# Optimization experiments

Measured on AMD Instinct MI355X. Metric: run time of the kernel, lower is better.

Reference implementation:

```python
import jax, jax.numpy as jnp
import numpy as np

N, E, F = 25000, 200000, 128


def setup_inputs() -> dict:
    key = jax.random.key(0)
    k1, k2, k3, k4 = jax.random.split(key, 4)
    x = jax.random.normal(k1, (N, F), dtype=jnp.float32)
    edge_index = jax.random.randint(k2, (2, E), 0, N, dtype=jnp.int32)
    batch = jnp.zeros((N,), dtype=jnp.int32)  # single graph
    # EdgePooling.lin = Linear(2F, 1); split weight into src/dst halves
    w_src = jax.random.normal(k3, (F,), dtype=jnp.float32) / np.sqrt(2.0 * F)
    w_dst = jax.random.normal(k4, (F,), dtype=jnp.float32) / np.sqrt(2.0 * F)
    b = jnp.zeros((1,), dtype=jnp.float32)
    return {"x": x, "edge_index": edge_index, "batch": batch,
            "w_src": w_src, "w_dst": w_dst, "b": b}


def reference(x, edge_index, batch, w_src, w_dst, b):
    src, dst = edge_index[0], edge_index[1]
    n = x.shape[0]
    # raw edge score: lin(cat(x[src], x[dst])) == x[src]@w_src + x[dst]@w_dst + b
    raw = x[src] @ w_src + x[dst] @ w_dst + b[0]                 # [E]
    # compute_edge_score_softmax: softmax over edges grouped by dst node
    m = jax.ops.segment_max(raw, dst, num_segments=n)
    z = jnp.exp(raw - m[dst])
    denom = jax.ops.segment_sum(z, dst, num_segments=n)
    e = z / denom[dst] + 0.5                                      # add_to_edge_score=0.5

    # greedy non-overlapping edge contraction, highest score first
    order = jnp.argsort(-e)
    src_s, dst_s, e_s = src[order], dst[order], e[order]

    def step(carry, st):
        matched, cluster, cnt = carry
        s, t = st
        ok = jnp.logical_not(matched[s] | matched[t])
        matched = matched.at[s].set(matched[s] | ok)
        matched = matched.at[t].set(matched[t] | ok)
        cluster = cluster.at[s].set(jnp.where(ok, cnt, cluster[s]))
        cluster = cluster.at[t].set(jnp.where(ok, cnt, cluster[t]))
        out = (ok, jnp.where(ok, cnt, n))  # n = sentinel (dropped later)
        cnt = cnt + ok.astype(cnt.dtype)
        return (matched, cluster, cnt), out

    init = (jnp.zeros((n,), bool), jnp.zeros((n,), jnp.int32), jnp.int32(0))
    (matched, cluster, cnt), (chosen, assigned) = jax.lax.scan(step, init, (src_s, dst_s))

    # leftover (unmatched) nodes become singleton clusters with consecutive ids
    left = jnp.logical_not(matched)
    cluster = jnp.where(left, cnt + jnp.cumsum(left.astype(jnp.int32)) - 1, cluster)
    num_clusters = cnt + left.sum()

    # per-cluster gating score: merged-edge score for pairs, 1.0 for singletons
    cscore = jnp.ones((n,), x.dtype).at[assigned].set(e_s, mode='drop')
    # new node features (padded to n rows; rows >= num_clusters are zero)
    new_x = jax.ops.segment_sum(x, cluster, num_segments=n) * cscore[:, None]
    new_batch = jnp.zeros((n,), batch.dtype).at[cluster].set(batch)
    new_ei = cluster[edge_index]
    new_ei = jnp.where(new_ei[0] == new_ei[1], -1, new_ei)  # mark self-loops invalid
    return new_x, new_ei, new_batch, num_clusters
```

## Files before the change

### kernel.cpp

```cpp
#include <hip/hip_runtime.h>
#include <stdint.h>

typedef unsigned int u32;
typedef unsigned long long u64;
typedef unsigned short u16;
typedef unsigned char u8;

#define FDIM  128
#define NNODE 25000
#define WG    1024
#define RB    64
#define EPT   16
#define RCHUNK (RB*EPT)
#define KBITS 18
#define RMASK ((1u << KBITS) - 1u)
#define TAG(r) (((0x3FFFu - (u32)(r)) << KBITS))
#define PRROUNDS 4
#define CB 256
#define CEPT 4
#define CCHUNK (CB*CEPT)
#define HST (256*200)
#define SCCH 1024

__device__ __forceinline__ u32 enc_f32(float f){
  u32 u = __float_as_uint(f);
  return (u & 0x80000000u) ? ~u : (u | 0x80000000u);
}
__device__ __forceinline__ float dec_f32(u32 u){
  u = (u & 0x80000000u) ? (u ^ 0x80000000u) : ~u;
  return __uint_as_float(u);
}

__device__ __forceinline__ float xla_expf(float x){
  x = fminf(x,  88.3762626647950f);
  x = fmaxf(x, -88.3762626647949f);
  float fx = floorf(fmaf(x, 1.44269504088896341f, 0.5f));
  float tmp = __fmul_rn(fx, 0.693359375f);
  float zz  = __fmul_rn(fx, -2.12194440e-4f);
  x = __fsub_rn(x, tmp);
  x = __fsub_rn(x, zz);
  float z2 = __fmul_rn(x, x);
  float y = fmaf(1.9875691500E-4f, x, 1.3981999507E-3f);
  y = fmaf(y, x, 8.3334519073E-3f);
  y = fmaf(y, x, 4.1665795894E-2f);
  y = fmaf(y, x, 1.6666665459E-1f);
  y = fmaf(y, x, 5.0000001201E-1f);
  y = fmaf(y, z2, x);
  y = __fadd_rn(y, 1.0f);
  int n = (int)fx;
  float p2n = __uint_as_float((u32)(n + 127) << 23);
  return __fmul_rn(y, p2n);
}

__global__ __launch_bounds__(256) void k_dots(const float* __restrict__ x,
                      const float* __restrict__ wsrc, const float* __restrict__ wdst,
                      float* __restrict__ ds, float* __restrict__ dd, int N_)
{
  __shared__ float4 w4[64];
  int t = threadIdx.x;
  if (t < 32) w4[t] = ((const float4*)wsrc)[t];
  else if (t < 64) w4[t] = ((const float4*)wdst)[t - 32];
  __syncthreads();
  int v = blockIdx.x * blockDim.x + t;
  if (v >= N_) return;
  const float4* xr = (const float4*)(x + (size_t)v * FDIM);
  float accs = 0.f, accd = 0.f;
  #pragma unroll 4
  for (int k = 0; k < 32; ++k) {
    float4 xv = xr[k], w = w4[k], u = w4[k + 32];
    accs = __fadd_rn(accs, __fmul_rn(xv.x, w.x));
    accs = __fadd_rn(accs, __fmul_rn(xv.y, w.y));
    accs = __fadd_rn(accs, __fmul_rn(xv.z, w.z));
    accs = __fadd_rn(accs, __fmul_rn(xv.w, w.w));
    accd = __fadd_rn(accd, __fmul_rn(xv.x, u.x));
    accd = __fadd_rn(accd, __fmul_rn(xv.y, u.y));
    accd = __fadd_rn(accd, __fmul_rn(xv.z, u.z));
    accd = __fadd_rn(accd, __fmul_rn(xv.w, u.w));
  }
  ds[v] = accs; dd[v] = accd;
}

__global__ __launch_bounds__(RB) void k_rawE(const int* __restrict__ ei, const float* __restrict__ ds,
                       const float* __restrict__ dd, const float* __restrict__ bia,
                       float* __restrict__ raw, u32* __restrict__ m_enc,
                       u64* __restrict__ kvA, u32* __restrict__ hist, int nb, int E_)
{
  __shared__ u32 h[256];
  int t = threadIdx.x, b = blockIdx.x;
  for (int i = t; i < 256; i += RB) h[i] = 0;
  __syncthreads();
  int lo = b * RCHUNK + t * EPT;
  int hi = lo + EPT; if (hi > E_) hi = E_;
  float bv = bia[0];
  for (int e = lo; e < hi; ++e) {
    int s = ei[e], d = ei[E_ + e];
    float r = __fadd_rn(__fadd_rn(ds[s], dd[d]), bv);
    raw[e] = r;
    atomicMax(&m_enc[d], enc_f32(r));
    kvA[e] = ((u64)(u32)d << 32) | (u32)e;
    atomicAdd(&h[(u32)d & 255u], 1u);
  }
  __syncthreads();
  for (int i = t; i < 256; i += RB) hist[(size_t)i * nb + b] = h[i];
}

__global__ __launch_bounds__(RB) void k_rhist(const u64* __restrict__ kv, u32* __restrict__ hist,
                                              int n, int nb, int shift)
{
  __shared__ u32 h[256];
  int t = threadIdx.x, b = blockIdx.x;
  for (int i = t; i < 256; i += RB) h[i] = 0;
  __syncthreads();
  int lo = b * RCHUNK + t * EPT;
  int hi = lo + EPT; if (hi > n) hi = n;
  for (int i = lo; i < hi; ++i) atomicAdd(&h[((u32)(kv[i] >> 32) >> shift) & 255u], 1u);
  __syncthreads();
  for (int i = t; i < 256; i += RB) hist[(size_t)i * nb + b] = h[i];
}

__global__ __launch_bounds__(256) void k_mbs1(const u32* __restrict__ a, u32* __restrict__ bsum, int m)
{
  __shared__ u32 sh[256];
  int t = threadIdx.x, b = blockIdx.x;
  int base = b * SCCH;
  u32 s = 0;
  #pragma unroll
  for (int k = 0; k < SCCH / 256; ++k) { int i = base + t + k * 256; if (i < m) s += a[i]; }
  sh[t] = s; __syncthreads();
  for (int off = 128; off > 0; off >>= 1) { if (t < off) sh[t] += sh[t + off]; __syncthreads(); }
  if (t == 0) bsum[b] = sh[0];
}

__global__ __launch_bounds__(256) void k_mbs3(u32* __restrict__ a, const u32* __restrict__ bsum, int m)
{
  __shared__ u32 sh[256];
  __shared__ u32 s_off;
  const int W = SCCH / 256;
  int t = threadIdx.x, b = blockIdx.x;
  sh[t] = (t < b) ? bsum[t] : 0u;
  __syncthreads();
  for (int off = 128; off > 0; off >>= 1) { if (t < off) sh[t] += sh[t + off]; __syncthreads(); }
  if (t == 0) s_off = sh[0];
  __syncthreads();
  int lo = b * SCCH + t * W;
  u32 v[W];
  u32 c = 0;
  #pragma unroll
  for (int k = 0; k < W; ++k) { int i = lo + k; v[k] = (i < m) ? a[i] : 0u; c += v[k]; }
  u32 mine = c;
  sh[t] = c; __syncthreads();
  for (int off = 1; off < 256; off <<= 1) {
    u32 x = (t >= off) ? sh[t - off] : 0u; __syncthreads();
    sh[t] += x; __syncthreads();
  }
  u32 run = s_off + sh[t] - mine;
  #pragma unroll
  for (int k = 0; k < W; ++k) { int i = lo + k; if (i < m) { a[i] = run; run += v[k]; } }
}

__global__ __launch_bounds__(RB) void k_rscat(const u64* __restrict__ kvin, u64* __restrict__ kvout,
                                              const u32* __restrict__ base, int n, int nb, int shift)
{
  __shared__ u16 h[RB][258];
  __shared__ u32 gbase[256];
  int t = threadIdx.x, b = blockIdx.x;
  for (int i = t; i < RB * 258 / 2; i += RB) ((u32*)h)[i] = 0u;
  __syncthreads();
  int lo = b * RCHUNK + t * EPT;
  int hi = lo + EPT; if (hi > n) hi = n;
  for (int i = lo; i < hi; ++i) { u32 d = ((u32)(kvin[i] >> 32) >> shift) & 255u; h[t][d]++; }
  __syncthreads();
  for (int dg = t; dg < 256; dg += RB) {
    u32 run = 0;
    for (int q = 0; q < RB; ++q) { u16 c = h[q][dg]; h[q][dg] = (u16)run; run += c; }
    gbase[dg] = base[(size_t)dg * nb + b];
  }
  __syncthreads();
  for (int i = lo; i < hi; ++i) {
    u64 kv = kvin[i];
    u32 d = ((u32)(kv >> 32) >> shift) & 255u;
    u32 p = gbase[d] + (u32)h[t][d];
    h[t][d]++;
    kvout[p] = kv;
  }
}

__global__ __launch_bounds__(RB) void k_rscatP(const u64* __restrict__ kvin,
                                               const u32* __restrict__ base, int n, int nb, int shift,
                                               u32* __restrict__ pairByRank, float* __restrict__ scoreByRank,
                                               u8* __restrict__ chosen, u32* __restrict__ nmin)
{
  __shared__ u16 h[RB][258];
  __shared__ u32 gbase[256];
  int t = threadIdx.x, b = blockIdx.x;
  for (int i = t; i < RB * 258 / 2; i += RB) ((u32*)h)[i] = 0u;
  __syncthreads();
  int lo = b * RCHUNK + t * EPT;
  int hi = lo + EPT; if (hi > n) hi = n;
  for (int i = lo; i < hi; ++i) { u32 d = ((u32)(kvin[i] >> 32) >> shift) & 255u; h[t][d]++; }
  __syncthreads();
  for (int dg = t; dg < 256; dg += RB) {
    u32 run = 0;
    for (int q = 0; q < RB; ++q) { u16 c = h[q][dg]; h[q][dg] = (u16)run; run += c; }
    gbase[dg] = base[(size_t)dg * nb + b];
  }
  __syncthreads();
  for (int i = lo; i < hi; ++i) {
    u64 kv = kvin[i];
    u32 key = (u32)(kv >> 32);
    u32 d = (key >> shift) & 255u;
    u32 p = gbase[d] + (u32)h[t][d];
    h[t][d]++;
    u32 sd = (u32)kv;
    pairByRank[p] = sd;
    scoreByRank[p] = dec_f32(~key);
    chosen[p] = 0;
    u32 val = TAG(0) | p;
    atomicMin(&nmin[sd >> 16], val);
    atomicMin(&nmin[sd & 0xFFFFu], val);
  }
}

__global__ void k_scores_seg(const u64* __restrict__ kvS, const float* __restrict__ raw,
                             const u32* __restrict__ m_enc, float* __restrict__ score, int E_)
{
  int i = blockIdx.x * blockDim.x + threadIdx.x;
  if (i >= E_) return;
  u32 d = (u32)(kvS[i] >> 32);
  if (i > 0 && (u32)(kvS[i - 1] >> 32) == d) return;
  float m = dec_f32(m_enc[d]);
  float denom = 0.f;
  int j = i;
  while (j < E_) {
    u64 kv = kvS[j];
    if ((u32)(kv >> 32) != d) break;
    denom = __fadd_rn(denom, xla_expf(__fsub_rn(raw[(u32)kv], m)));
    ++j;
  }
  for (int q = i; q < j; ++q) {
    u32 e = (u32)kvS[q];
    float z = xla_expf(__fsub_rn(raw[e], m));
    score[e] = __fadd_rn(__fdiv_rn(z, denom), 0.5f);
  }
}

__global__ __launch_bounds__(RB) void k_key_score(const float* __restrict__ score, const int* __restrict__ ei,
                            u64* __restrict__ kvB, u32* __restrict__ hist, int nb, int E_)
{
  __shared__ u32 h[256];
  int t = threadIdx.x, b = blockIdx.x;
  for (int i = t; i < 256; i += RB) h[i] = 0;
  __syncthreads();
  int lo = b * RCHUNK + t * EPT;
  int hi = lo + EPT; if (hi > E_) hi = E_;
  for (int e = lo; e < hi; ++e) {
    u32 key = ~enc_f32(score[e]);
    u32 sd = ((u32)ei[e] << 16) | (u32)ei[E_ + e];
    kvB[e] = ((u64)key << 32) | sd;
    atomicAdd(&h[key & 255u], 1u);
  }
  __syncthreads();
  for (int i = t; i < 256; i += RB) hist[(size_t)i * nb + b] = h[i];
}

__global__ void k_choose0N(const u32* __restrict__ pairByRank, const u32* __restrict__ nmin,
                           u8* __restrict__ chosen, u8* __restrict__ matched_g, int N_)
{
  int v = blockIdx.x * blockDim.x + threadIdx.x;
  if (v >= N_) return;
  u32 mv = nmin[v];
  if (mv == 0xFFFFFFFFu) return;
  u32 k = mv & RMASK;
  u32 sd = pairByRank[k];
  u32 s = sd >> 16, d = sd & 0xFFFFu;
  u32 other = ((u32)v == s) ? d : s;
  if (nmin[other] == mv) {
    matched_g[v] = 1;
    if ((u32)v == s) chosen[k] = 1;
  }
}

__global__ void k_compact0(const u32* __restrict__ pairByRank, const u8* __restrict__ matched_g,
                           u64* __restrict__ liveOut, u32* __restrict__ nmin,
                           u32* __restrict__ nlive, int E_)
{
  int k = blockIdx.x * blockDim.x + threadIdx.x;
  int lane = threadIdx.x & 63;
  bool liveE = false; u32 s = 0, d = 0;
  if (k < E_) {
    u32 sd = pairByRank[k];
    s = sd >> 16; d = sd & 0xFFFFu;
    liveE = (!matched_g[s] && !matched_g[d]);
  }
  u64 m = __ballot(liveE);
  if (m != 0ull) {
    int leader = __ffsll((long long)m) - 1;
    u32 base = 0;
    if (lane == leader) base = atomicAdd(nlive, (u32)__popcll(m));
    base = (u32)__shfl((int)base, leader);
    if (liveE) {
      u32 pfx = (u32)__popcll(m & ((1ull << lane) - 1ull));
      liveOut[base + pfx] = ((u64)(u32)k << 32) | ((u64)s << 16) | (u64)d;
      u32 nval = TAG(1) | (u32)k;
      atomicMin(&nmin[s], nval);
      atomicMin(&nmin[d], nval);
    }
  }
}

__global__ void k_chooseR(const u64* __restrict__ liveIn, const u32* __restrict__ nliveIn,
                          const u32* __restrict__ nmin,
                          u8* __restrict__ chosen, u8* __restrict__ matched_g, u32 rtag)
{
  u32 i = blockIdx.x * blockDim.x + threadIdx.x;
  if (i >= *nliveIn) return;
  u64 v = liveIn[i];
  u32 k = (u32)(v >> 32), s = ((u32)v) >> 16, d = (u32)v & 0xFFFFu;
  u32 myval = rtag | k;
  if (nmin[s] == myval && nmin[d] == myval) { chosen[k] = 1; matched_g[s] = 1; matched_g[d] = 1; }
}

__global__ void k_compactR(const u64* __restrict__ liveIn, const u32* __restrict__ nliveIn,
                           const u8* __restrict__ matched_g,
                           u64* __restrict__ liveOut, u32* __restrict__ nmin,
                           u32* __restrict__ nliveOut, u32 ntag)
{
  u32 i = blockIdx.x * blockDim.x + threadIdx.x;
  int lane = threadIdx.x & 63;
  bool liveE = false; u64 v = 0; u32 s = 0, d = 0;
  if (i < *nliveIn) {
    v = liveIn[i];
    s = ((u32)v) >> 16; d = (u32)v & 0xFFFFu;
    liveE = (!matched_g[s] && !matched_g[d]);
  }
  u64 m = __ballot(liveE);
  if (m != 0ull) {
    int leader = __ffsll((long long)m) - 1;
    u32 base = 0;
    if (lane == leader) base = atomicAdd(nliveOut, (u32)__popcll(m));
    base = (u32)__shfl((int)base, leader);
    if (liveE) {
      u32 pfx = (u32)__popcll(m & ((1ull << lane) - 1ull));
      liveOut[base + pfx] = v;
      u32 nval = ntag | (u32)(v >> 32);
      atomicMin(&nmin[s], nval);
      atomicMin(&nmin[d], nval);
    }
  }
}

__global__ __launch_bounds__(WG) void k_match(
    u64* liveA, u64* liveB, const u32* __restrict__ nmin_g, u8* __restrict__ matched_g,
    const u32* __restrict__ nliveIn, u8* __restrict__ chosen, int N_)
{
  __shared__ u32 node_min[NNODE];
  __shared__ u32 s_nlive, s_next;
  const int t = threadIdx.x;
  const int lane = t & 63;

  for (int i = t; i < N_; i += WG) node_min[i] = matched_g[i] ? 0u : nmin_g[i];
  if (t == 0) { s_nlive = *nliveIn; s_next = 0u; }
  __syncthreads();

  u64* LA = liveA; u64* LB = liveB;
  u32 r = PRROUNDS;
  while (true) {
    u32 nl = s_nlive;
    if (nl == 0u || r > 16000u) break;
    const u32 tag  = TAG(r);
    const u32 ntag = TAG(r + 1);

    for (u32 i = (u32)t; i < nl; i += WG) {
      u64 v = LA[i];
      u32 k = (u32)(v >> 32);
      u32 s = ((u32)v) >> 16, d = (u32)v & 0xFFFFu;
      u32 myval = tag | k;
      if (node_min[s] == myval && node_min[d] == myval) {
        chosen[k] = 1; node_min[s] = 0u; node_min[d] = 0u;
      }
    }
    __syncthreads();

    for (u32 i0 = (u32)(t & ~63); i0 < nl; i0 += WG) {
      u32 i = i0 + (u32)lane;
      bool liveE = false; u64 v = 0;
      u32 s = 0, d = 0;
      if (i < nl) {
        v = LA[i];
        s = ((u32)v) >> 16; d = (u32)v & 0xFFFFu;
        liveE = (node_min[s] != 0u && node_min[d] != 0u);
      }
      u64 m = __ballot(liveE);
      if (m != 0ull) {
        int leader = __ffsll((long long)m) - 1;
        u32 baseIdx = 0;
        if (lane == leader) baseIdx = atomicAdd(&s_next, (u32)__popcll(m));
        baseIdx = (u32)__shfl((int)baseIdx, leader);
        if (liveE) {
          u32 pfx = (u32)__popcll(m & ((1ull << lane) - 1ull));
          LB[baseIdx + pfx] = v;
          u32 nval = ntag | (u32)(v >> 32);
          atomicMin(&node_min[s], nval);
          atomicMin(&node_min[d], nval);
        }
      }
    }
    __syncthreads();
    if (t == 0) { s_nlive = s_next; s_next = 0u; }
    { u64* tmp = LA; LA = LB; LB = tmp; }
    ++r;
    __syncthreads();
  }

  for (int i = t; i < N_; i += WG) matched_g[i] = (node_min[i] == 0u) ? 1 : 0;
}

__global__ __launch_bounds__(CB) void k_sums(const u8* __restrict__ chosen, u32* __restrict__ csum, int E_,
                                             const u8* __restrict__ matched, u32* __restrict__ nsum, int N_,
                                             int nbc)
{
  __shared__ u32 sh[CB];
  int t = threadIdx.x, b = blockIdx.x;
  const u8* src; int n; u32* dst; int bb;
  if (b < nbc) { src = chosen; n = E_; dst = csum; bb = b; }
  else         { src = matched; n = N_; dst = nsum; bb = b - nbc; }
  int lo = bb * CCHUNK + t * CEPT;
  int hi = lo + CEPT; if (hi > n) hi = n;
  u32 c = 0;
  if (b < nbc) { for (int i = lo; i < hi; ++i) c += src[i]; }
  else         { for (int i = lo; i < hi; ++i) c += (src[i] ? 0u : 1u); }
  sh[t] = c; __syncthreads();
  for (int off = CB / 2; off > 0; off >>= 1) { if (t < off) sh[t] += sh[t + off]; __syncthreads(); }
  if (t == 0) dst[bb] = sh[0];
}

__global__ __launch_bounds__(CB) void k_assign(const u8* __restrict__ chosen, const u32* __restrict__ csum,
    const u32* __restrict__ pairByRank, const float* __restrict__ scoreByRank, int E_,
    const u8* __restrict__ matched, const u32* __restrict__ nsum, int N_,
    u32* __restrict__ cnts,
    int* __restrict__ cluster, u32* __restrict__ pairA, u32* __restrict__ pairB,
    float* __restrict__ cscore, int nbc, int nbn)
{
  __shared__ u32 sh[CB];
  __shared__ u32 s_off;
  int t = threadIdx.x, b = blockIdx.x;
  if (b < nbc) {
    sh[t] = (t < b) ? csum[t] : 0u;
    __syncthreads();
    for (int off = CB / 2; off > 0; off >>= 1) { if (t < off) sh[t] += sh[t + off]; __syncthreads(); }
    if (t == 0) s_off = sh[0];
    __syncthreads();
    int lo = b * CCHUNK + t * CEPT;
    int hi = lo + CEPT; if (hi > E_) hi = E_;
    u32 c = 0;
    for (int i = lo; i < hi; ++i) c += chosen[i];
    u32 mine = c;
    sh[t] = c; __syncthreads();
    for (int off = 1; off < CB; off <<= 1) {
      u32 a = (t >= off) ? sh[t - off] : 0u; __syncthreads();
      sh[t] += a; __syncthreads();
    }
    u32 run = s_off + sh[t] - mine;
    for (int i = lo; i < hi; ++i) {
      if (chosen[i]) {
        u32 cc = run++;
        u32 sd = pairByRank[i];
        u32 sv = sd >> 16, dv = sd & 0xFFFFu;
        cluster[sv] = (int)cc; cluster[dv] = (int)cc;
        pairA[cc] = sv; pairB[cc] = dv; cscore[cc] = scoreByRank[i];
      }
    }
  } else {
    int bb = b - nbc;
    sh[t] = ((t < nbc) ? csum[t] : 0u) + ((t >= nbc && t < nbc + bb) ? nsum[t - nbc] : 0u);
    __syncthreads();
    for (int off = CB / 2; off > 0; off >>= 1) { if (t < off) sh[t] += sh[t + off]; __syncthreads(); }
    if (t == 0) s_off = sh[0];
    __syncthreads();
    if (bb == 0) {
      sh[t] = ((t < nbc) ? csum[t] : 0u) + ((t >= nbc && t < nbc + nbn) ? nsum[t - nbc] : 0u);
      __syncthreads();
      for (int off = CB / 2; off > 0; off >>= 1) { if (t < off) sh[t] += sh[t + off]; __syncthreads(); }
      if (t == 0) cnts[3] = sh[0];
      __syncthreads();
    }
    int lo = bb * CCHUNK + t * CEPT;
    int hi = lo + CEPT; if (hi > N_) hi = N_;
    u32 c = 0;
    for (int i = lo; i < hi; ++i) c += (matched[i] ? 0u : 1u);
    u32 mine = c;
    sh[t] = c; __syncthreads();
    for (int off = 1; off < CB; off <<= 1) {
      u32 a = (t >= off) ? sh[t - off] : 0u; __syncthreads();
      sh[t] += a; __syncthreads();
    }
    u32 run = s_off + sh[t] - mine;
    for (int v = lo; v < hi; ++v) {
      if (!matched[v]) {
        u32 cc = run++;
        cluster[v] = (int)cc;
        pairA[cc] = (u32)v; pairB[cc] = (u32)v; cscore[cc] = 1.0f;
      }
    }
  }
}

__global__ __launch_bounds__(256) void k_out(const float* __restrict__ x, const u32* __restrict__ pairA,
                     const u32* __restrict__ pairB, const float* __restrict__ cscore,
                     const u32* __restrict__ cnts,
                     const int* __restrict__ ei, const int* __restrict__ cluster,
                     float* __restrict__ out, int N_, int E_, int nxb)
{
  int b = blockIdx.x, t = threadIdx.x;
  if (b < nxb) {
    int j = b * 256 + t;
    int total = N_ * (FDIM / 4);
    if (j >= total) return;
    u32 c = (u32)(j >> 5);
    int q = (j & 31) * 4;
    float4 o;
    if (c >= cnts[3]) {
      o.x = 0.f; o.y = 0.f; o.z = 0.f; o.w = 0.f;
    } else {
      u32 a = pairA[c], bb = pairB[c];
      float cs = cscore[c];
      const float4 va = *(const float4*)(x + (size_t)a * FDIM + q);
      if (a == bb) {
        o.x = __fmul_rn(va.x, cs); o.y = __fmul_rn(va.y, cs);
        o.z = __fmul_rn(va.z, cs); o.w = __fmul_rn(va.w, cs);
      } else {
        const float4 vb = *(const float4*)(x + (size_t)bb * FDIM + q);
        o.x = __fmul_rn(__fadd_rn(va.x, vb.x), cs);
        o.y = __fmul_rn(__fadd_rn(va.y, vb.y), cs);
        o.z = __fmul_rn(__fadd_rn(va.z, vb.z), cs);
        o.w = __fmul_rn(__fadd_rn(va.w, vb.w), cs);
      }
    }
    *(float4*)(out + (size_t)c * FDIM + q) = o;
  } else {
    int e = (b - nxb) * 256 + t;
    if (e >= E_) return;
    int c0 = cluster[ei[e]];
    int c1 = cluster[ei[E_ + e]];
    if (c0 == c1) { c0 = -1; c1 = -1; }
    size_t base = (size_t)N_ * FDIM;
    out[base + e] = (float)c0;
    out[base + E_ + e] = (float)c1;
    if (e < N_) out[base + 2 * (size_t)E_ + e] = 0.0f;
    if (e == 0) out[base + 2 * (size_t)E_ + N_] = (float)cnts[3];
  }
}

extern "C" void kernel_launch(void* const* d_in, const int* in_sizes, int n_in,
                              void* d_out, int out_size, void* d_ws, size_t ws_size,
                              hipStream_t stream)
{
  const float* x    = (const float*)d_in[0];
  const int*   ei   = (const int*)d_in[1];
  const float* wsrc = (const float*)d_in[3];
  const float* wdst = (const float*)d_in[4];
  const float* b    = (const float*)d_in[5];
  const int N = in_sizes[0] / FDIM;
  const int E = in_sizes[1] / 2;

  u32* w = (u32*)d_ws;
  float* raw   = (float*)w;      w += E;
  float* score = (float*)w;      w += E;
  u64* kvA = (u64*)w;            w += 2 * E;
  u64* kvB = (u64*)w;            w += 2 * E;
  float* ds = (float*)w;         w += N;
  float* dd = (float*)w;         w += N;
  int* cluster = (int*)w;        w += N;
  u32* pairA = w;                w += N;
  u32* pairB = w;                w += N;
  float* cscore = (float*)w;     w += N;
  u32* nmin = w;                 w += N;
  u32* csum = w;                 w += 256;
  u32* nsum = w;                 w += 64;
  u32* bsum = w;                 w += 256;
  u32* hist = w;                 w += HST;
  u32* zeros = w;
  u32* m_enc  = w;               w += N;
  u8*  matched_g = (u8*)w;       w += (N + 3) / 4;
  u32* cnts = w;                 w += 16;
  size_t zwords = (size_t)(w - zeros);

  u64* liveA = (u64*)d_out;
  u64* liveB = (u64*)((u32*)d_out + 2 * (size_t)E);
  u32* pairByRank  = (u32*)d_out + 4 * (size_t)E;
  float* scoreByRank = (float*)((u32*)d_out + 5 * (size_t)E);
  u8* chosen = (u8*)((u32*)d_out + 6 * (size_t)E);

  const int TB = 256;
  const int gridE = (E + TB - 1) / TB;
  const int gridN = (N + TB - 1) / TB;
  const int nb = (E + RCHUNK - 1) / RCHUNK;
  const int m  = nb * 256;
  const int nsb = (m + SCCH - 1) / SCCH;
  const int nbc = (E + CCHUNK - 1) / CCHUNK;
  const int nbn = (N + CCHUNK - 1) / CCHUNK;
  const int nxb = (N * (FDIM / 4) + TB - 1) / TB;

  hipMemsetAsync(zeros, 0, zwords * 4, stream);
  hipMemsetAsync(nmin, 0xFF, (size_t)N * 4, stream);

  #define HSCAN() do { \
    k_mbs1<<<nsb, 256, 0, stream>>>(hist, bsum, m); \
    k_mbs3<<<nsb, 256, 0, stream>>>(hist, bsum, m); \
  } while (0)

  k_dots<<<gridN, TB, 0, stream>>>(x, wsrc, wdst, ds, dd, N);
  k_rawE<<<nb, RB, 0, stream>>>(ei, ds, dd, b, raw, m_enc, kvA, hist, nb, E);

  HSCAN();
  k_rscat<<<nb, RB, 0, stream>>>(kvA, kvB, hist, E, nb, 0);
  k_rhist<<<nb, RB, 0, stream>>>(kvB, hist, E, nb, 8);
  HSCAN();
  k_rscat<<<nb, RB, 0, stream>>>(kvB, kvA, hist, E, nb, 8);

  k_scores_seg<<<gridE, TB, 0, stream>>>(kvA, raw, m_enc, score, E);

  k_key_score<<<nb, RB, 0, stream>>>(score, ei, kvB, hist, nb, E);
  HSCAN();
  k_rscat<<<nb, RB, 0, stream>>>(kvB, kvA, hist, E, nb, 0);
  k_rhist<<<nb, RB, 0, stream>>>(kvA, hist, E, nb, 8);
  HSCAN();
  k_rscat<<<nb, RB, 0, stream>>>(kvA, kvB, hist, E, nb, 8);
  k_rhist<<<nb, RB, 0, stream>>>(kvB, hist, E, nb, 16);
  HSCAN();
  k_rscatP<<<nb, RB, 0, stream>>>(kvB, hist, E, nb, 16,
                                  pairByRank, scoreByRank, chosen, nmin);

  k_choose0N<<<gridN, TB, 0, stream>>>(pairByRank, nmin, chosen, matched_g, N);
  k_compact0<<<gridE, TB, 0, stream>>>(pairByRank, matched_g, liveB, nmin, &cnts[8], E);

  u64* Lin = liveB; u64* Lout = liveA;
  for (int r = 1; r < PRROUNDS; ++r) {
    k_chooseR<<<gridE, TB, 0, stream>>>(Lin, &cnts[8 + r - 1], nmin, chosen, matched_g, TAG(r));
    k_compactR<<<gridE, TB, 0, stream>>>(Lin, &cnts[8 + r - 1], matched_g, Lout, nmin,
                                         &cnts[8 + r], TAG(r + 1));
    u64* tmp = Lin; Lin = Lout; Lout = tmp;
  }

  k_match<<<1, WG, 0, stream>>>(Lin, Lout, nmin, matched_g, &cnts[8 + PRROUNDS - 1],
                                chosen, N);

  k_sums<<<nbc + nbn, CB, 0, stream>>>(chosen, csum, E, matched_g, nsum, N, nbc);
  k_assign<<<nbc + nbn, CB, 0, stream>>>(chosen, csum, pairByRank, scoreByRank, E,
                                         matched_g, nsum, N, cnts,
                                         cluster, pairA, pairB, cscore, nbc, nbn);

  k_out<<<nxb + gridE, TB, 0, stream>>>(x, pairA, pairB, cscore, cnts, ei, cluster,
                                        (float*)d_out, N, E, nxb);
}
```

Measured before the change: 338.0 us.

## Replace two-pass histogram scan with per-digit totals and single-pass base kernel

Histogram kernels now also accumulate per-digit global totals with atomics, so the radix base offsets can be computed by one kernel (one block per digit scanning across blocks) instead of a two-kernel scan. This removes one launch per radix pass. The nmin and m_enc initialisation moves into k_dots, which drops a memset, and m_enc leaves the zeroed region. The cost is extra global atomics on 256 counters per histogram block, and the new scan assumes nb is at most 256.

After: 343.2 us. No clear change (+1.5%).

```diff
diff --git a/kernel.cpp b/kernel.cpp
--- a/kernel.cpp
+++ b/kernel.cpp
@@ -20,7 +20,6 @@
 #define CEPT 4
 #define CCHUNK (CB*CEPT)
 #define HST (256*200)
-#define SCCH 1024
 
 __device__ __forceinline__ u32 enc_f32(float f){
   u32 u = __float_as_uint(f);
@@ -54,7 +53,8 @@
 
 __global__ __launch_bounds__(256) void k_dots(const float* __restrict__ x,
                       const float* __restrict__ wsrc, const float* __restrict__ wdst,
-                      float* __restrict__ ds, float* __restrict__ dd, int N_)
+                      float* __restrict__ ds, float* __restrict__ dd,
+                      u32* __restrict__ nmin, u32* __restrict__ m_enc, int N_)
 {
   __shared__ float4 w4[64];
   int t = threadIdx.x;
@@ -63,6 +63,8 @@
   __syncthreads();
   int v = blockIdx.x * blockDim.x + t;
   if (v >= N_) return;
+  nmin[v] = 0xFFFFFFFFu;
+  m_enc[v] = 0u;
   const float4* xr = (const float4*)(x + (size_t)v * FDIM);
   float accs = 0.f, accd = 0.f;
   #pragma unroll 4
@@ -83,7 +85,8 @@
 __global__ __launch_bounds__(RB) void k_rawE(const int* __restrict__ ei, const float* __restrict__ ds,
                        const float* __restrict__ dd, const float* __restrict__ bia,
                        float* __restrict__ raw, u32* __restrict__ m_enc,
-                       u64* __restrict__ kvA, u32* __restrict__ hist, int nb, int E_)
+                       u64* __restrict__ kvA, u32* __restrict__ hist, u32* __restrict__ dtot,
+                       int nb, int E_)
 {
   __shared__ u32 h[256];
   int t = threadIdx.x, b = blockIdx.x;
@@ -101,11 +104,11 @@
     atomicAdd(&h[(u32)d & 255u], 1u);
   }
   __syncthreads();
-  for (int i = t; i < 256; i += RB) hist[(size_t)i * nb + b] = h[i];
+  for (int i = t; i < 256; i += RB) { u32 c = h[i]; hist[(size_t)i * nb + b] = c; if (c) atomicAdd(&dtot[i], c); }
 }
 
 __global__ __launch_bounds__(RB) void k_rhist(const u64* __restrict__ kv, u32* __restrict__ hist,
-                                              int n, int nb, int shift)
+                                              u32* __restrict__ dtot, int n, int nb, int shift)
 {
   __shared__ u32 h[256];
   int t = threadIdx.x, b = blockIdx.x;
@@ -115,47 +118,26 @@
   int hi = lo + EPT; if (hi > n) hi = n;
   for (int i = lo; i < hi; ++i) atomicAdd(&h[((u32)(kv[i] >> 32) >> shift) & 255u], 1u);
   __syncthreads();
-  for (int i = t; i < 256; i += RB) hist[(size_t)i * nb + b] = h[i];
-}
-
-__global__ __launch_bounds__(256) void k_mbs1(const u32* __restrict__ a, u32* __restrict__ bsum, int m)
+  for (int i = t; i < 256; i += RB) { u32 c = h[i]; hist[(size_t)i * nb + b] = c; if (c) atomicAdd(&dtot[i], c); }
+}
+
+__global__ __launch_bounds__(256) void k_rbase(u32* __restrict__ hist, const u32* __restrict__ dtot, int nb)
 {
   __shared__ u32 sh[256];
-  int t = threadIdx.x, b = blockIdx.x;
-  int base = b * SCCH;
-  u32 s = 0;
-  #pragma unroll
-  for (int k = 0; k < SCCH / 256; ++k) { int i = base + t + k * 256; if (i < m) s += a[i]; }
-  sh[t] = s; __syncthreads();
+  __shared__ u32 s_doff;
+  int t = threadIdx.x, dg = blockIdx.x;
+  sh[t] = (t < dg) ? dtot[t] : 0u;
+  __syncthreads();
   for (int off = 128; off > 0; off >>= 1) { if (t < off) sh[t] += sh[t + off]; __syncthreads(); }
-  if (t == 0) bsum[b] = sh[0];
-}
-
-__global__ __launch_bounds__(256) void k_mbs3(u32* __restrict__ a, const u32* __restrict__ bsum, int m)
-{
-  __shared__ u32 sh[256];
-  __shared__ u32 s_off;
-  const int W = SCCH / 256;
-  int t = threadIdx.x, b = blockIdx.x;
-  sh[t] = (t < b) ? bsum[t] : 0u;
-  __syncthreads();
-  for (int off = 128; off > 0; off >>= 1) { if (t < off) sh[t] += sh[t + off]; __syncthreads(); }
-  if (t == 0) s_off = sh[0];
-  __syncthreads();
-  int lo = b * SCCH + t * W;
-  u32 v[W];
-  u32 c = 0;
-  #pragma unroll
-  for (int k = 0; k < W; ++k) { int i = lo + k; v[k] = (i < m) ? a[i] : 0u; c += v[k]; }
-  u32 mine = c;
-  sh[t] = c; __syncthreads();
+  if (t == 0) s_doff = sh[0];
+  __syncthreads();
+  u32 v = (t < nb) ? hist[(size_t)dg * nb + t] : 0u;
+  sh[t] = v; __syncthreads();
   for (int off = 1; off < 256; off <<= 1) {
-    u32 x = (t >= off) ? sh[t - off] : 0u; __syncthreads();
-    sh[t] += x; __syncthreads();
-  }
-  u32 run = s_off + sh[t] - mine;
-  #pragma unroll
-  for (int k = 0; k < W; ++k) { int i = lo + k; if (i < m) { a[i] = run; run += v[k]; } }
+    u32 a = (t >= off) ? sh[t - off] : 0u; __syncthreads();
+    sh[t] += a; __syncthreads();
+  }
+  if (t < nb) hist[(size_t)dg * nb + t] = s_doff + sh[t] - v;
 }
 
 __global__ __launch_bounds__(RB) void k_rscat(const u64* __restrict__ kvin, u64* __restrict__ kvout,
@@ -245,7 +227,8 @@
 }
 
 __global__ __launch_bounds__(RB) void k_key_score(const float* __restrict__ score, const int* __restrict__ ei,
-                            u64* __restrict__ kvB, u32* __restrict__ hist, int nb, int E_)
+                            u64* __restrict__ kvB, u32* __restrict__ hist, u32* __restrict__ dtot,
+                            int nb, int E_)
 {
   __shared__ u32 h[256];
   int t = threadIdx.x, b = blockIdx.x;
@@ -260,7 +243,7 @@
     atomicAdd(&h[key & 255u], 1u);
   }
   __syncthreads();
-  for (int i = t; i < 256; i += RB) hist[(size_t)i * nb + b] = h[i];
+  for (int i = t; i < 256; i += RB) { u32 c = h[i]; hist[(size_t)i * nb + b] = c; if (c) atomicAdd(&dtot[i], c); }
 }
 
 __global__ void k_choose0N(const u32* __restrict__ pairByRank, const u32* __restrict__ nmin,
@@ -575,14 +558,18 @@
   u32* pairB = w;                w += N;
   float* cscore = (float*)w;     w += N;
   u32* nmin = w;                 w += N;
+  u32* m_enc = w;                w += N;
   u32* csum = w;                 w += 256;
   u32* nsum = w;                 w += 64;
-  u32* bsum = w;                 w += 256;
   u32* hist = w;                 w += HST;
   u32* zeros = w;
-  u32* m_enc  = w;               w += N;
   u8*  matched_g = (u8*)w;       w += (N + 3) / 4;
   u32* cnts = w;                 w += 16;
+  u32* dt_d0 = w;                w += 256;
+  u32* dt_d1 = w;                w += 256;
+  u32* dt_s0 = w;                w += 256;
+  u32* dt_s1 = w;                w += 256;
+  u32* dt_s2 = w;                w += 256;
   size_t zwords = (size_t)(w - zeros);
 
   u64* liveA = (u64*)d_out;
@@ -595,39 +582,31 @@
   const int gridE = (E + TB - 1) / TB;
   const int gridN = (N + TB - 1) / TB;
   const int nb = (E + RCHUNK - 1) / RCHUNK;
-  const int m  = nb * 256;
-  const int nsb = (m + SCCH - 1) / SCCH;
   const int nbc = (E + CCHUNK - 1) / CCHUNK;
   const int nbn = (N + CCHUNK - 1) / CCHUNK;
   const int nxb = (N * (FDIM / 4) + TB - 1) / TB;
 
   hipMemsetAsync(zeros, 0, zwords * 4, stream);
-  hipMemsetAsync(nmin, 0xFF, (size_t)N * 4, stream);
-
-  #define HSCAN() do { \
-    k_mbs1<<<nsb, 256, 0, stream>>>(hist, bsum, m); \
-    k_mbs3<<<nsb, 256, 0, stream>>>(hist, bsum, m); \
-  } while (0)
-
-  k_dots<<<gridN, TB, 0, stream>>>(x, wsrc, wdst, ds, dd, N);
-  k_rawE<<<nb, RB, 0, stream>>>(ei, ds, dd, b, raw, m_enc, kvA, hist, nb, E);
-
-  HSCAN();
+
+  k_dots<<<gridN, TB, 0, stream>>>(x, wsrc, wdst, ds, dd, nmin, m_enc, N);
+  k_rawE<<<nb, RB, 0, stream>>>(ei, ds, dd, b, raw, m_enc, kvA, hist, dt_d0, nb, E);
+
+  k_rbase<<<256, 256, 0, stream>>>(hist, dt_d0, nb);
   k_rscat<<<nb, RB, 0, stream>>>(kvA, kvB, hist, E, nb, 0);
-  k_rhist<<<nb, RB, 0, stream>>>(kvB, hist, E, nb, 8);
-  HSCAN();
+  k_rhist<<<nb, RB, 0, stream>>>(kvB, hist, dt_d1, E, nb, 8);
+  k_rbase<<<256, 256, 0, stream>>>(hist, dt_d1, nb);
   k_rscat<<<nb, RB, 0, stream>>>(kvB, kvA, hist, E, nb, 8);
 
   k_scores_seg<<<gridE, TB, 0, stream>>>(kvA, raw, m_enc, score, E);
 
-  k_key_score<<<nb, RB, 0, stream>>>(score, ei, kvB, hist, nb, E);
-  HSCAN();
+  k_key_score<<<nb, RB, 0, stream>>>(score, ei, kvB, hist, dt_s0, nb, E);
+  k_rbase<<<256, 256, 0, stream>>>(hist, dt_s0, nb);
   k_rscat<<<nb, RB, 0, stream>>>(kvB, kvA, hist, E, nb, 0);
-  k_rhist<<<nb, RB, 0, stream>>>(kvA, hist, E, nb, 8);
-  HSCAN();
+  k_rhist<<<nb, RB, 0, stream>>>(kvA, hist, dt_s1, E, nb, 8);
+  k_rbase<<<256, 256, 0, stream>>>(hist, dt_s1, nb);
   k_rscat<<<nb, RB, 0, stream>>>(kvA, kvB, hist, E, nb, 8);
-  k_rhist<<<nb, RB, 0, stream>>>(kvB, hist, E, nb, 16);
-  HSCAN();
+  k_rhist<<<nb, RB, 0, stream>>>(kvB, hist, dt_s2, E, nb, 16);
+  k_rbase<<<256, 256, 0, stream>>>(hist, dt_s2, nb);
   k_rscatP<<<nb, RB, 0, stream>>>(kvB, hist, E, nb, 16,
                                   pairByRank, scoreByRank, chosen, nmin);
 
```
